# Kernel optimization log

Hardware: AMD Instinct MI355X
Metric: run time of the kernel (lower is better)

The kernel has to match this reference:

```python
import jax, jax.numpy as jnp
import numpy as np

B, S, D = 4, 2048, 1024
E, ES, K = 16, 256, 4  # n_experts, expert_size, top-k (= n_heads)
STD_GATE = 0.02


def setup_inputs() -> dict:
    key = jax.random.key(0)
    k1, k2, k3, k4 = jax.random.split(key, 4)
    x = jax.random.normal(k1, (B, S, D), dtype=jnp.float32)
    # init per module: gate ~ N(0, d^-0.5), keys ~ N(0, d^-0.5), values ~ N(0, size^-0.5)
    w_gate = jax.random.normal(k2, (E, D), dtype=jnp.float32) * (D ** -0.5)
    keys = jax.random.normal(k3, (E, D, ES), dtype=jnp.float32) * (D ** -0.5)
    values = jax.random.normal(k4, (E, ES, D), dtype=jnp.float32) * ((E * ES) ** -0.5)
    return {"x": x, "w_gate": w_gate, "keys": keys, "values": values}


def reference(x, w_gate, keys, values):
    # sigma-MoE forward (selection_mode='sigmoid', activation=relu,
    # num_selected = n_heads = K, no bias, no dropout, eval mode)
    xt = x.reshape(-1, D)                         # [T, D]
    T = xt.shape[0]
    logits = xt @ w_gate.T                        # [T, E]
    sel = jax.nn.sigmoid(logits)                  # sigmoid gating
    sel_val, sel_idx = jax.lax.top_k(sel, K)      # [T, K]
    # sparse gate weights as dense [T, E] mask (zeros for unselected experts)
    gate_w = jnp.zeros((T, E), dtype=x.dtype).at[
        jnp.arange(T)[:, None], sel_idx
    ].set(sel_val)
    # per-expert hidden: h[t,e,s] = relu(sum_d x[t,d] keys[e,d,s])
    h = jax.nn.relu(jnp.einsum('td,eds->tes', xt, keys))  # [T, E, ES]
    # weighted scatter back through values: out = sum_e gate * h_e @ values_e
    out = jnp.einsum('tes,te,esv->tv', h, gate_w, values)  # [T, D]
    return out.reshape(B, S, D)
```

## Files before the change

kernel.cpp:

```cpp
#include <hip/hip_runtime.h>
#include <hip/hip_bf16.h>
#include <stdint.h>

#define T_TOK 8192
#define DIM   1024
#define NEXP  16
#define ESZ   256
#define TOPK  4
#define BM    128
#define BK    64
#define NPAIR (T_TOK*TOPK)
#define NBLK  128
#define MAXROWS (T_TOK*TOPK + NEXP*BM)
#define MAXTILES (T_TOK*TOPK/BM + NEXP)

typedef __hip_bfloat16 bf16;
typedef short bf16x8 __attribute__((ext_vector_type(8)));
typedef float f32x4 __attribute__((ext_vector_type(4)));

__device__ __forceinline__ unsigned short f2bu(float f){
  __hip_bfloat16 b = __float2bfloat16(f);
  return *reinterpret_cast<unsigned short*>(&b);
}
__device__ __forceinline__ float bu2f(unsigned short u){
  __hip_bfloat16 b = *reinterpret_cast<__hip_bfloat16*>(&u);
  return __bfloat162float(b);
}

__device__ __forceinline__ void gload16(const void* g, void* l){
  __builtin_amdgcn_global_load_lds((const __attribute__((address_space(1))) void*)g,
                                   (__attribute__((address_space(3))) void*)l, 16, 0, 0);
}

__global__ __launch_bounds__(256) void k_gate(const float* __restrict__ x,
    const float* __restrict__ wg, bf16* __restrict__ xb,
    int* __restrict__ sel_idx, float* __restrict__ sel_gate)
{
  const int wave = threadIdx.x >> 6, lane = threadIdx.x & 63;
  const int t = blockIdx.x*4 + wave;
  const float* xr = x + (size_t)t*DIM;
  float4 xv[4];
#pragma unroll
  for (int c=0;c<4;c++) xv[c] = *(const float4*)(xr + c*256 + lane*4);
#pragma unroll
  for (int c=0;c<4;c++){
    ushort4 o; o.x=f2bu(xv[c].x); o.y=f2bu(xv[c].y); o.z=f2bu(xv[c].z); o.w=f2bu(xv[c].w);
    *(ushort4*)((unsigned short*)xb + (size_t)t*DIM + c*256 + lane*4) = o;
  }
  float sg[NEXP];
#pragma unroll
  for (int e=0;e<NEXP;e++){
    const float* wr = wg + e*DIM;
    float p = 0.f;
#pragma unroll
    for (int c=0;c<4;c++){
      float4 w = *(const float4*)(wr + c*256 + lane*4);
      p += xv[c].x*w.x + xv[c].y*w.y + xv[c].z*w.z + xv[c].w*w.w;
    }
#pragma unroll
    for (int s=1;s<64;s<<=1) p += __shfl_xor(p, s);
    sg[e] = 1.f/(1.f + expf(-p));
  }
  if (lane==0){
    unsigned chosen = 0;
#pragma unroll
    for (int k=0;k<TOPK;k++){
      float best=-1.f; int bi=0;
#pragma unroll
      for (int e=0;e<NEXP;e++){
        float v = ((chosen>>e)&1u) ? -2.f : sg[e];
        if (v>best){best=v;bi=e;}
      }
      chosen |= 1u<<bi;
      sel_idx[t*TOPK+k]=bi; sel_gate[t*TOPK+k]=best;
    }
  }
}

__global__ __launch_bounds__(256) void k_transpose(const float* __restrict__ in,
    bf16* __restrict__ out, int R, int C)
{
  __shared__ float tile[32][33];
  const float* src = in + (size_t)blockIdx.z*R*C;
  bf16* dst = out + (size_t)blockIdx.z*R*C;
  int tx = threadIdx.x & 31, ty = threadIdx.x >> 5;
  int r0 = blockIdx.y*32, c0 = blockIdx.x*32;
#pragma unroll
  for (int i=0;i<4;i++){ int r = ty + i*8; tile[r][tx] = src[(size_t)(r0+r)*C + c0 + tx]; }
  __syncthreads();
#pragma unroll
  for (int i=0;i<4;i++){ int r = ty + i*8; dst[(size_t)(c0+r)*R + r0 + tx] = __float2bfloat16(tile[tx][r]); }
}

__global__ __launch_bounds__(256) void k_hist(const int* __restrict__ sel_idx,
    int* __restrict__ block_hist)
{
  __shared__ int h[NEXP];
  if (threadIdx.x < NEXP) h[threadIdx.x]=0;
  __syncthreads();
  atomicAdd(&h[sel_idx[blockIdx.x*256 + threadIdx.x]], 1);
  __syncthreads();
  if (threadIdx.x < NEXP) block_hist[blockIdx.x*NEXP + threadIdx.x] = h[threadIdx.x];
}

__global__ void k_meta(const int* __restrict__ block_hist,
    int* __restrict__ tile_expert, int* __restrict__ tile_rowstart,
    int* __restrict__ tile_segend, int* __restrict__ block_base)
{
  __shared__ int cnt[NEXP], seg[NEXP];
  const int tid = threadIdx.x;
  if (tid < NEXP){
    int s=0;
    for (int b=0;b<NBLK;b++) s += block_hist[b*NEXP + tid];
    cnt[tid]=s;
  }
  __syncthreads();
  if (tid==0){
    int off=0, tc=0;
    for (int e=0;e<NEXP;e++){
      seg[e]=off;
      int c = cnt[e];
      int nt = (c + BM - 1)/BM;
      for (int i=0;i<nt;i++){
        tile_expert[tc]=e; tile_rowstart[tc]=off+i*BM; tile_segend[tc]=off+c; tc++;
      }
      off += nt*BM;
    }
    for (; tc<MAXTILES; tc++) tile_expert[tc]=-1;
  }
  __syncthreads();
  if (tid < NEXP){
    int s = seg[tid];
    for (int b=0;b<NBLK;b++){ block_base[b*NEXP + tid] = s; s += block_hist[b*NEXP + tid]; }
  }
}

__global__ __launch_bounds__(256) void k_scatter(const int* __restrict__ sel_idx,
    const float* __restrict__ sel_gate, const int* __restrict__ block_base,
    int* __restrict__ assign_token, float* __restrict__ assign_gate,
    int* __restrict__ inv_rows)
{
  __shared__ int wcnt[4][NEXP];
  const int p = blockIdx.x*256 + threadIdx.x;
  const int wave = threadIdx.x >> 6, lane = threadIdx.x & 63;
  const int e = sel_idx[p];
  const float g = sel_gate[p];
  int rank = 0;
#pragma unroll
  for (int ee=0; ee<NEXP; ee++){
    unsigned long long m = __ballot(e==ee);
    if (lane==0) wcnt[wave][ee] = (int)__popcll(m);
    if (e==ee) rank = (int)__popcll(m & ((1ull<<lane)-1ull));
  }
  __syncthreads();
  int pre = 0;
  for (int w=0; w<wave; w++) pre += wcnt[w][e];
  const int row = block_base[blockIdx.x*NEXP + e] + pre + rank;
  assign_token[row] = p >> 2;
  assign_gate[row]  = g;
  inv_rows[p] = row;
}

__global__ __launch_bounds__(256) void k_gemm1(
    const bf16* __restrict__ xb, const bf16* __restrict__ kT,
    const int* __restrict__ assign_token, const float* __restrict__ assign_gate,
    const int* __restrict__ tile_expert, const int* __restrict__ tile_rowstart,
    const int* __restrict__ tile_segend, bf16* __restrict__ h)
{
  __shared__ char smem[BM*BK*2*2];
  __shared__ int   tokens_s[BM];
  __shared__ float gates_s[BM];

  const int tile = blockIdx.x, nb = blockIdx.y;
  const int e = tile_expert[tile];
  if (e < 0) return;
  const int row0 = tile_rowstart[tile];
  const int segend = tile_segend[tile];
  const int tid = threadIdx.x, wave = tid>>6, lane = tid&63;

  if (tid < BM){
    int rg = row0 + tid;
    bool vld = rg < segend;
    tokens_s[tid] = vld ? assign_token[rg] : 0;
    gates_s[tid]  = vld ? assign_gate[rg] : 0.f;
  }
  __syncthreads();

  char* As = smem; char* Bs = smem + BM*BK*2;
  const bf16* gA[4]; const bf16* gB[4]; char* lA[4]; char* lB[4];
#pragma unroll
  for (int i=0;i<4;i++){
    int rl = (wave*4+i)*8 + (lane>>3);
    int c  = (lane&7) ^ (rl&7);
    gA[i] = xb + (size_t)tokens_s[rl]*DIM + c*8;
    lA[i] = As + (wave*4+i)*1024;
    gB[i] = kT + ((size_t)e*ESZ + nb*BM + rl)*DIM + c*8;
    lB[i] = Bs + (wave*4+i)*1024;
  }

  f32x4 acc[4][4];
#pragma unroll
  for (int m=0;m<4;m++)
#pragma unroll
    for (int n=0;n<4;n++) acc[m][n] = {0.f,0.f,0.f,0.f};

  const int wr0 = (wave>>1)*64, wc0 = (wave&1)*64;

  for (int kt=0; kt<DIM/BK; ++kt){
#pragma unroll
    for (int i=0;i<4;i++){ gload16(gA[i] + kt*BK, lA[i]); gload16(gB[i] + kt*BK, lB[i]); }
    asm volatile("s_waitcnt vmcnt(0)" ::: "memory");
    __syncthreads();
#pragma unroll
    for (int kk=0;kk<2;kk++){
      bf16x8 af[4], bfr[4];
#pragma unroll
      for (int m=0;m<4;m++){
        int row = wr0 + m*16 + (lane&15);
        int kb  = kk*64 + (lane>>4)*16;
        af[m] = *(const bf16x8*)(As + row*128 + (kb ^ ((row&7)<<4)));
      }
#pragma unroll
      for (int n=0;n<4;n++){
        int col = wc0 + n*16 + (lane&15);
        int kb  = kk*64 + (lane>>4)*16;
        bfr[n] = *(const bf16x8*)(Bs + col*128 + (kb ^ ((col&7)<<4)));
      }
#pragma unroll
      for (int m=0;m<4;m++)
#pragma unroll
        for (int n=0;n<4;n++)
          acc[m][n] = __builtin_amdgcn_mfma_f32_16x16x32_bf16(af[m], bfr[n], acc[m][n], 0,0,0);
    }
    __syncthreads();
  }

#pragma unroll
  for (int m=0;m<4;m++)
#pragma unroll
    for (int n=0;n<4;n++){
      int col = wc0 + n*16 + (lane&15);
#pragma unroll
      for (int j=0;j<4;j++){
        int rloc = wr0 + m*16 + ((lane>>4)<<2) + j;
        float v = fmaxf(acc[m][n][j], 0.f) * gates_s[rloc];
        h[(size_t)(row0 + rloc)*ESZ + nb*BM + col] = __float2bfloat16(v);
      }
    }
}

__global__ __launch_bounds__(256) void k_gemm2(
    const bf16* __restrict__ h, const bf16* __restrict__ vT,
    const int* __restrict__ tile_expert, const int* __restrict__ tile_rowstart,
    bf16* __restrict__ partial)
{
  __shared__ char smem[BM*BK*2*2];

  const int tile = blockIdx.x, nb = blockIdx.y;
  const int e = tile_expert[tile];
  if (e < 0) return;
  const int row0 = tile_rowstart[tile];
  const int tid = threadIdx.x, wave = tid>>6, lane = tid&63;

  char* As = smem; char* Bs = smem + BM*BK*2;
  const bf16* gA[4]; const bf16* gB[4]; char* lA[4]; char* lB[4];
#pragma unroll
  for (int i=0;i<4;i++){
    int rl = (wave*4+i)*8 + (lane>>3);
    int c  = (lane&7) ^ (rl&7);
    gA[i] = h + (size_t)(row0 + rl)*ESZ + c*8;
    lA[i] = As + (wave*4+i)*1024;
    gB[i] = vT + ((size_t)e*DIM + nb*BM + rl)*ESZ + c*8;
    lB[i] = Bs + (wave*4+i)*1024;
  }

  f32x4 acc[4][4];
#pragma unroll
  for (int m=0;m<4;m++)
#pragma unroll
    for (int n=0;n<4;n++) acc[m][n] = {0.f,0.f,0.f,0.f};

  const int wr0 = (wave>>1)*64, wc0 = (wave&1)*64;

  for (int kt=0; kt<ESZ/BK; ++kt){
#pragma unroll
    for (int i=0;i<4;i++){ gload16(gA[i] + kt*BK, lA[i]); gload16(gB[i] + kt*BK, lB[i]); }
    asm volatile("s_waitcnt vmcnt(0)" ::: "memory");
    __syncthreads();
#pragma unroll
    for (int kk=0;kk<2;kk++){
      bf16x8 af[4], bfr[4];
#pragma unroll
      for (int m=0;m<4;m++){
        int row = wr0 + m*16 + (lane&15);
        int kb  = kk*64 + (lane>>4)*16;
        af[m] = *(const bf16x8*)(As + row*128 + (kb ^ ((row&7)<<4)));
      }
#pragma unroll
      for (int n=0;n<4;n++){
        int col = wc0 + n*16 + (lane&15);
        int kb  = kk*64 + (lane>>4)*16;
        bfr[n] = *(const bf16x8*)(Bs + col*128 + (kb ^ ((col&7)<<4)));
      }
#pragma unroll
      for (int m=0;m<4;m++)
#pragma unroll
        for (int n=0;n<4;n++)
          acc[m][n] = __builtin_amdgcn_mfma_f32_16x16x32_bf16(af[m], bfr[n], acc[m][n], 0,0,0);
    }
    __syncthreads();
  }

#pragma unroll
  for (int m=0;m<4;m++)
#pragma unroll
    for (int n=0;n<4;n++){
      int col = wc0 + n*16 + (lane&15);
#pragma unroll
      for (int j=0;j<4;j++){
        int rloc = wr0 + m*16 + ((lane>>4)<<2) + j;
        partial[(size_t)(row0 + rloc)*DIM + nb*BM + col] = __float2bfloat16(acc[m][n][j]);
      }
    }
}

__global__ __launch_bounds__(256) void k_reduce(const bf16* __restrict__ partial,
    const int* __restrict__ inv_rows, float* __restrict__ out)
{
  const int t = blockIdx.x;
  const int c0 = threadIdx.x * 4;
  int rows[TOPK];
#pragma unroll
  for (int k=0;k<TOPK;k++) rows[k] = inv_rows[t*TOPK+k];
  float a0=0.f,a1=0.f,a2=0.f,a3=0.f;
#pragma unroll
  for (int k=0;k<TOPK;k++){
    ushort4 v = *(const ushort4*)((const unsigned short*)partial + (size_t)rows[k]*DIM + c0);
    a0 += bu2f(v.x); a1 += bu2f(v.y); a2 += bu2f(v.z); a3 += bu2f(v.w);
  }
  float4 o = {a0,a1,a2,a3};
  *(float4*)(out + (size_t)t*DIM + c0) = o;
}

extern "C" void kernel_launch(void* const* d_in, const int* in_sizes, int n_in,
                              void* d_out, int out_size, void* d_ws, size_t ws_size,
                              hipStream_t stream)
{
  const float* x      = (const float*)d_in[0];
  const float* wg     = (const float*)d_in[1];
  const float* keys   = (const float*)d_in[2];
  const float* values = (const float*)d_in[3];
  float* out = (float*)d_out;

  char* ws = (char*)d_ws;
  size_t off = 0;
  bf16* vT   = (bf16*)(ws+off); off += (size_t)NEXP*DIM*ESZ*2;
  bf16* hbuf = (bf16*)(ws+off); off += (size_t)MAXROWS*ESZ*2;
  int*   sel_idx      = (int*)  (ws+off); off += (size_t)NPAIR*4;
  float* sel_gate     = (float*)(ws+off); off += (size_t)NPAIR*4;
  int*   assign_token = (int*)  (ws+off); off += (size_t)MAXROWS*4;
  float* assign_gate  = (float*)(ws+off); off += (size_t)MAXROWS*4;
  int*   inv_rows     = (int*)  (ws+off); off += (size_t)NPAIR*4;
  int*   block_hist   = (int*)  (ws+off); off += (size_t)NBLK*NEXP*4;
  int*   block_base   = (int*)  (ws+off); off += (size_t)NBLK*NEXP*4;
  int*   tile_expert  = (int*)  (ws+off); off += 4096;
  int*   tile_rowstart= (int*)  (ws+off); off += 4096;
  int*   tile_segend  = (int*)  (ws+off); off += 4096;
  const size_t PARTIAL_BYTES = (size_t)MAXROWS*DIM*2;
  const size_t XB_BYTES = (size_t)T_TOK*DIM*2;
  const size_t KT_BYTES = (size_t)NEXP*ESZ*DIM*2;
  bf16* partial = (bf16*)(ws+off); off += PARTIAL_BYTES;
  bf16* xb = (bf16*)((char*)partial + PARTIAL_BYTES - XB_BYTES - KT_BYTES);
  bf16* kT = (bf16*)((char*)partial + PARTIAL_BYTES - KT_BYTES);

  k_gate<<<T_TOK/4, 256, 0, stream>>>(x, wg, xb, sel_idx, sel_gate);
  k_transpose<<<dim3(ESZ/32, DIM/32, NEXP), 256, 0, stream>>>(keys, kT, DIM, ESZ);
  k_transpose<<<dim3(DIM/32, ESZ/32, NEXP), 256, 0, stream>>>(values, vT, ESZ, DIM);
  k_hist<<<NBLK, 256, 0, stream>>>(sel_idx, block_hist);
  k_meta<<<1, 256, 0, stream>>>(block_hist, tile_expert, tile_rowstart, tile_segend, block_base);
  k_scatter<<<NBLK, 256, 0, stream>>>(sel_idx, sel_gate, block_base, assign_token,
      assign_gate, inv_rows);
  k_gemm1<<<dim3(MAXTILES, ESZ/BM), 256, 0, stream>>>(xb, kT, assign_token, assign_gate,
      tile_expert, tile_rowstart, tile_segend, hbuf);
  k_gemm2<<<dim3(MAXTILES, DIM/BM), 256, 0, stream>>>(hbuf, vT,
      tile_expert, tile_rowstart, partial);
  k_reduce<<<T_TOK, 256, 0, stream>>>(partial, inv_rows, out);
}
```

Before: 161.4 us.

## Double-buffer LDS tiles in expert GEMMs, swap grid order, fuse transposes

Both grouped GEMM kernels now use two LDS buffers and prefetch the next K tile while computing the current one. A partial vmcnt wait replaces the full drain each iteration, so global loads overlap MFMA work. The grid axes are swapped so blocks sharing a row tile (and its gathered A rows) are adjacent, which should improve L2 reuse. The two weight transposes are merged into one launch. Doubling LDS to 64KB per block may lower occupancy.

```diff
diff --git a/kernel.cpp b/kernel.cpp
--- a/kernel.cpp
+++ b/kernel.cpp
@@ -77,14 +77,17 @@
   }
 }
 
-__global__ __launch_bounds__(256) void k_transpose(const float* __restrict__ in,
-    bf16* __restrict__ out, int R, int C)
+__global__ __launch_bounds__(256) void k_transpose2(const float* __restrict__ keys,
+    const float* __restrict__ values, bf16* __restrict__ kT, bf16* __restrict__ vT)
 {
   __shared__ float tile[32][33];
-  const float* src = in + (size_t)blockIdx.z*R*C;
-  bf16* dst = out + (size_t)blockIdx.z*R*C;
-  int tx = threadIdx.x & 31, ty = threadIdx.x >> 5;
-  int r0 = blockIdx.y*32, c0 = blockIdx.x*32;
+  const int which = blockIdx.y >> 4, e = blockIdx.y & 15;
+  const int R = which ? ESZ : DIM, C = which ? DIM : ESZ;
+  const float* src = (which ? values : keys) + (size_t)e*DIM*ESZ;
+  bf16* dst = (which ? vT : kT) + (size_t)e*DIM*ESZ;
+  const int ctiles = C/32;
+  const int r0 = (blockIdx.x / ctiles)*32, c0 = (blockIdx.x % ctiles)*32;
+  const int tx = threadIdx.x & 31, ty = threadIdx.x >> 5;
 #pragma unroll
   for (int i=0;i<4;i++){ int r = ty + i*8; tile[r][tx] = src[(size_t)(r0+r)*C + c0 + tx]; }
   __syncthreads();
@@ -167,11 +170,11 @@
     const int* __restrict__ tile_expert, const int* __restrict__ tile_rowstart,
     const int* __restrict__ tile_segend, bf16* __restrict__ h)
 {
-  __shared__ char smem[BM*BK*2*2];
+  __shared__ char smem[65536];
   __shared__ int   tokens_s[BM];
   __shared__ float gates_s[BM];
 
-  const int tile = blockIdx.x, nb = blockIdx.y;
+  const int nb = blockIdx.x, tile = blockIdx.y;
   const int e = tile_expert[tile];
   if (e < 0) return;
   const int row0 = tile_rowstart[tile];
@@ -186,16 +189,16 @@
   }
   __syncthreads();
 
-  char* As = smem; char* Bs = smem + BM*BK*2;
-  const bf16* gA[4]; const bf16* gB[4]; char* lA[4]; char* lB[4];
+  char* As = smem;
+  char* Bs = smem + 32768;
+  const bf16* gA[4]; const bf16* gB[4]; int lo[4];
 #pragma unroll
   for (int i=0;i<4;i++){
     int rl = (wave*4+i)*8 + (lane>>3);
     int c  = (lane&7) ^ (rl&7);
     gA[i] = xb + (size_t)tokens_s[rl]*DIM + c*8;
-    lA[i] = As + (wave*4+i)*1024;
     gB[i] = kT + ((size_t)e*ESZ + nb*BM + rl)*DIM + c*8;
-    lB[i] = Bs + (wave*4+i)*1024;
+    lo[i] = (wave*4+i)*1024;
   }
 
   f32x4 acc[4][4];
@@ -205,12 +208,26 @@
     for (int n=0;n<4;n++) acc[m][n] = {0.f,0.f,0.f,0.f};
 
   const int wr0 = (wave>>1)*64, wc0 = (wave&1)*64;
-
-  for (int kt=0; kt<DIM/BK; ++kt){
-#pragma unroll
-    for (int i=0;i<4;i++){ gload16(gA[i] + kt*BK, lA[i]); gload16(gB[i] + kt*BK, lB[i]); }
-    asm volatile("s_waitcnt vmcnt(0)" ::: "memory");
+  const int NT = DIM/BK;
+
+#pragma unroll
+  for (int i=0;i<4;i++){ gload16(gA[i], As + lo[i]); gload16(gB[i], Bs + lo[i]); }
+
+  for (int kt=0; kt<NT; ++kt){
+    const int cur = kt & 1;
+    if (kt+1 < NT){
+      const int nxt = cur^1;
+#pragma unroll
+      for (int i=0;i<4;i++){
+        gload16(gA[i] + (kt+1)*BK, As + nxt*16384 + lo[i]);
+        gload16(gB[i] + (kt+1)*BK, Bs + nxt*16384 + lo[i]);
+      }
+      asm volatile("s_waitcnt vmcnt(8)" ::: "memory");
+    } else {
+      asm volatile("s_waitcnt vmcnt(0)" ::: "memory");
+    }
     __syncthreads();
+    const char* Ab = As + cur*16384; const char* Bb = Bs + cur*16384;
 #pragma unroll
     for (int kk=0;kk<2;kk++){
       bf16x8 af[4], bfr[4];
@@ -218,13 +235,13 @@
       for (int m=0;m<4;m++){
         int row = wr0 + m*16 + (lane&15);
         int kb  = kk*64 + (lane>>4)*16;
-        af[m] = *(const bf16x8*)(As + row*128 + (kb ^ ((row&7)<<4)));
+        af[m] = *(const bf16x8*)(Ab + row*128 + (kb ^ ((row&7)<<4)));
       }
 #pragma unroll
       for (int n=0;n<4;n++){
         int col = wc0 + n*16 + (lane&15);
         int kb  = kk*64 + (lane>>4)*16;
-        bfr[n] = *(const bf16x8*)(Bs + col*128 + (kb ^ ((col&7)<<4)));
+        bfr[n] = *(const bf16x8*)(Bb + col*128 + (kb ^ ((col&7)<<4)));
       }
 #pragma unroll
       for (int m=0;m<4;m++)
@@ -254,24 +271,24 @@
     const int* __restrict__ tile_expert, const int* __restrict__ tile_rowstart,
     bf16* __restrict__ partial)
 {
-  __shared__ char smem[BM*BK*2*2];
-
-  const int tile = blockIdx.x, nb = blockIdx.y;
+  __shared__ char smem[65536];
+
+  const int nb = blockIdx.x, tile = blockIdx.y;
   const int e = tile_expert[tile];
   if (e < 0) return;
   const int row0 = tile_rowstart[tile];
   const int tid = threadIdx.x, wave = tid>>6, lane = tid&63;
 
-  char* As = smem; char* Bs = smem + BM*BK*2;
-  const bf16* gA[4]; const bf16* gB[4]; char* lA[4]; char* lB[4];
+  char* As = smem;
+  char* Bs = smem + 32768;
+  const bf16* gA[4]; const bf16* gB[4]; int lo[4];
 #pragma unroll
   for (int i=0;i<4;i++){
     int rl = (wave*4+i)*8 + (lane>>3);
     int c  = (lane&7) ^ (rl&7);
     gA[i] = h + (size_t)(row0 + rl)*ESZ + c*8;
-    lA[i] = As + (wave*4+i)*1024;
     gB[i] = vT + ((size_t)e*DIM + nb*BM + rl)*ESZ + c*8;
-    lB[i] = Bs + (wave*4+i)*1024;
+    lo[i] = (wave*4+i)*1024;
   }
 
   f32x4 acc[4][4];
@@ -281,12 +298,26 @@
     for (int n=0;n<4;n++) acc[m][n] = {0.f,0.f,0.f,0.f};
 
   const int wr0 = (wave>>1)*64, wc0 = (wave&1)*64;
-
-  for (int kt=0; kt<ESZ/BK; ++kt){
-#pragma unroll
-    for (int i=0;i<4;i++){ gload16(gA[i] + kt*BK, lA[i]); gload16(gB[i] + kt*BK, lB[i]); }
-    asm volatile("s_waitcnt vmcnt(0)" ::: "memory");
+  const int NT = ESZ/BK;
+
+#pragma unroll
+  for (int i=0;i<4;i++){ gload16(gA[i], As + lo[i]); gload16(gB[i], Bs + lo[i]); }
+
+  for (int kt=0; kt<NT; ++kt){
+    const int cur = kt & 1;
+    if (kt+1 < NT){
+      const int nxt = cur^1;
+#pragma unroll
+      for (int i=0;i<4;i++){
+        gload16(gA[i] + (kt+1)*BK, As + nxt*16384 + lo[i]);
+        gload16(gB[i] + (kt+1)*BK, Bs + nxt*16384 + lo[i]);
+      }
+      asm volatile("s_waitcnt vmcnt(8)" ::: "memory");
+    } else {
+      asm volatile("s_waitcnt vmcnt(0)" ::: "memory");
+    }
     __syncthreads();
+    const char* Ab = As + cur*16384; const char* Bb = Bs + cur*16384;
 #pragma unroll
     for (int kk=0;kk<2;kk++){
       bf16x8 af[4], bfr[4];
@@ -294,13 +325,13 @@
       for (int m=0;m<4;m++){
         int row = wr0 + m*16 + (lane&15);
         int kb  = kk*64 + (lane>>4)*16;
-        af[m] = *(const bf16x8*)(As + row*128 + (kb ^ ((row&7)<<4)));
+        af[m] = *(const bf16x8*)(Ab + row*128 + (kb ^ ((row&7)<<4)));
       }
 #pragma unroll
       for (int n=0;n<4;n++){
         int col = wc0 + n*16 + (lane&15);
         int kb  = kk*64 + (lane>>4)*16;
-        bfr[n] = *(const bf16x8*)(Bs + col*128 + (kb ^ ((col&7)<<4)));
+        bfr[n] = *(const bf16x8*)(Bb + col*128 + (kb ^ ((col&7)<<4)));
       }
 #pragma unroll
       for (int m=0;m<4;m++)
@@ -374,15 +405,14 @@
   bf16* kT = (bf16*)((char*)partial + PARTIAL_BYTES - KT_BYTES);
 
   k_gate<<<T_TOK/4, 256, 0, stream>>>(x, wg, xb, sel_idx, sel_gate);
-  k_transpose<<<dim3(ESZ/32, DIM/32, NEXP), 256, 0, stream>>>(keys, kT, DIM, ESZ);
-  k_transpose<<<dim3(DIM/32, ESZ/32, NEXP), 256, 0, stream>>>(values, vT, ESZ, DIM);
+  k_transpose2<<<dim3(256, NEXP*2), 256, 0, stream>>>(keys, values, kT, vT);
   k_hist<<<NBLK, 256, 0, stream>>>(sel_idx, block_hist);
   k_meta<<<1, 256, 0, stream>>>(block_hist, tile_expert, tile_rowstart, tile_segend, block_base);
   k_scatter<<<NBLK, 256, 0, stream>>>(sel_idx, sel_gate, block_base, assign_token,
       assign_gate, inv_rows);
-  k_gemm1<<<dim3(MAXTILES, ESZ/BM), 256, 0, stream>>>(xb, kT, assign_token, assign_gate,
+  k_gemm1<<<dim3(ESZ/BM, MAXTILES), 256, 0, stream>>>(xb, kT, assign_token, assign_gate,
       tile_expert, tile_rowstart, tile_segend, hbuf);
-  k_gemm2<<<dim3(MAXTILES, DIM/BM), 256, 0, stream>>>(hbuf, vT,
+  k_gemm2<<<dim3(DIM/BM, MAXTILES), 256, 0, stream>>>(hbuf, vT,
       tile_expert, tile_rowstart, partial);
   k_reduce<<<T_TOK, 256, 0, stream>>>(partial, inv_rows, out);
 }
```

Result: slower. 167.4 us (+3.7%).
